# Optimization experiments

Hardware: AMD Instinct MI355X
Metric: run time of the kernel (lower is better)

Reference implementation:

```python
import jax, jax.numpy as jnp
import numpy as np

B, T, H, POOL, MAX_ITER = 32, 1024, 128, 16, 4
D = 2 * H  # feature size of U rows


def _maxout(x, w, b, out_dim, pool):
    # x: [..., fin], w: [fin, out_dim*pool], b: [out_dim*pool]
    y = x @ w + b
    y = y.reshape(y.shape[:-1] + (out_dim, pool))
    return y.max(axis=-1)


def _hmn(U, us, ue, h, WDw, WDb, W1w, W1b, W2w, W2b, W3w, W3b):
    # U: [B,T,2H]; us, ue: [B,2H]; h: [B,H] -> scores [B,T]
    r = jnp.tanh(jnp.concatenate([h, us, ue], axis=-1) @ WDw + WDb)  # [B,H]
    rt = jnp.broadcast_to(r[:, None, :], (U.shape[0], U.shape[1], r.shape[-1]))
    m1 = _maxout(jnp.concatenate([U, rt], axis=-1), W1w, W1b, H, POOL)  # [B,T,H]
    m2 = _maxout(m1, W2w, W2b, H, POOL)                                  # [B,T,H]
    m3 = _maxout(jnp.concatenate([m1, m2], axis=-1), W3w, W3b, 1, POOL)  # [B,T,1]
    return m3[..., 0]  # [B,T]


def _lstm_cell(x, h, c, wih, whh, bih, bhh):
    gates = x @ wih.T + bih + h @ whh.T + bhh  # [B,4H]
    i, f, g, o = jnp.split(gates, 4, axis=-1)
    i, f, o = jax.nn.sigmoid(i), jax.nn.sigmoid(f), jax.nn.sigmoid(o)
    g = jnp.tanh(g)
    c2 = f * c + i * g
    h2 = o * jnp.tanh(c2)
    return h2, c2


def setup_inputs() -> dict:
    key = jax.random.key(0)
    ks = jax.random.split(key, 24)
    s = 0.05
    gn = lambda k, shape: (jax.random.normal(k, shape, jnp.float32) * s)
    inp = {"U": jax.random.normal(ks[0], (B, T, D), jnp.float32)}
    for tag, off in (("s", 1), ("e", 9)):
        inp[f"WD{tag}_w"] = gn(ks[off + 0], (5 * H, H))
        inp[f"WD{tag}_b"] = jnp.zeros((H,), jnp.float32)
        inp[f"W1{tag}_w"] = gn(ks[off + 1], (3 * H, H * POOL))
        inp[f"W1{tag}_b"] = jnp.zeros((H * POOL,), jnp.float32)
        inp[f"W2{tag}_w"] = gn(ks[off + 2], (H, H * POOL))
        inp[f"W2{tag}_b"] = jnp.zeros((H * POOL,), jnp.float32)
        inp[f"W3{tag}_w"] = gn(ks[off + 3], (2 * H, POOL))
        inp[f"W3{tag}_b"] = jnp.zeros((POOL,), jnp.float32)
    inp["lstm_wih"] = gn(ks[20], (4 * H, 4 * H))
    inp["lstm_whh"] = gn(ks[21], (4 * H, H))
    inp["lstm_bih"] = jnp.zeros((4 * H,), jnp.float32)
    inp["lstm_bhh"] = jnp.zeros((4 * H,), jnp.float32)
    return inp


def reference(U,
              WDs_w, WDs_b, W1s_w, W1s_b, W2s_w, W2s_b, W3s_w, W3s_b,
              WDe_w, WDe_b, W1e_w, W1e_b, W2e_w, W2e_b, W3e_w, W3e_b,
              lstm_wih, lstm_whh, lstm_bih, lstm_bhh):
    b = U.shape[0]
    bidx = jnp.arange(b)
    h = jnp.zeros((b, H), U.dtype)
    c = jnp.zeros((b, H), U.dtype)
    us, ue = U[:, 0, :], U[:, 1, :]
    entropies = []
    for _ in range(MAX_ITER):  # training-mode: run all iterations (no host-sync early stop)
        alpha_sc = _hmn(U, us, ue, h, WDs_w, WDs_b, W1s_w, W1s_b, W2s_w, W2s_b, W3s_w, W3s_b)
        alpha = jnp.argmax(alpha_sc, axis=1)           # [B]
        us = U[bidx, alpha, :]                          # data-dependent gather
        beta_sc = _hmn(U, us, ue, h, WDe_w, WDe_b, W1e_w, W1e_b, W2e_w, W2e_b, W3e_w, W3e_b)
        beta = jnp.argmax(beta_sc, axis=1)
        ue = U[bidx, beta, :]
        h, c = _lstm_cell(jnp.concatenate([us, ue], axis=1), h, c,
                          lstm_wih, lstm_whh, lstm_bih, lstm_bhh)
        entropies.append(jnp.stack([alpha_sc, beta_sc], axis=0))
    ent = jnp.stack(entropies, axis=0)  # [max_iter, 2, B, T]
    return alpha, beta, ent
```

## Files before the change

kernel.cpp:

```cpp
#include <hip/hip_runtime.h>
#include <math.h>

static constexpr int cB = 32;
static constexpr int cT = 1024;
static constexpr int cH = 128;
static constexpr int cD = 256;
static constexpr int cN = 2048;
static constexpr int cM = cB * cT;

typedef __attribute__((ext_vector_type(8))) short short8;
typedef __attribute__((ext_vector_type(4))) float f32x4;

__device__ __forceinline__ ushort f2bf(float x) {
    union { float f; unsigned u; } v; v.f = x;
    unsigned r = v.u + 0x7FFF + ((v.u >> 16) & 1);
    return (ushort)(r >> 16);
}
__device__ __forceinline__ float bf2f(ushort h) {
    union { float f; unsigned u; } v; v.u = ((unsigned)h) << 16;
    return v.f;
}

__device__ __forceinline__ void gload_lds16(const ushort* g, ushort* l) {
    __builtin_amdgcn_global_load_lds(
        (const __attribute__((address_space(1))) unsigned int*)(const void*)g,
        (__attribute__((address_space(3))) unsigned int*)(void*)l,
        16, 0, 0);
}

template<int K, bool POOL, bool WRITE_HL>
__global__ __launch_bounds__(256, 2)
void mfma_gemm(const ushort* __restrict__ Ah, const ushort* __restrict__ Al,
               const ushort* __restrict__ Bth, const ushort* __restrict__ Btl,
               const float* __restrict__ initv, int init_bstride,
               float* __restrict__ out, ushort* __restrict__ outh,
               ushort* __restrict__ outl)
{
    __shared__ __attribute__((aligned(16))) ushort sAh[128 * 32];
    __shared__ __attribute__((aligned(16))) ushort sAl[128 * 32];
    __shared__ __attribute__((aligned(16))) ushort sBh[128 * 32];
    __shared__ __attribute__((aligned(16))) ushort sBl[128 * 32];

    const int tid  = threadIdx.x;
    const int wave = tid >> 6;
    const int lane = tid & 63;
    const int l15  = lane & 15;
    const int lg   = lane >> 4;
    const int wr   = wave >> 1;
    const int wc   = wave & 1;
    const int m0   = blockIdx.y * 128;
    const int n0   = blockIdx.x * 128;
    const int brow = m0 >> 10;

    float iv[4] = {0.f, 0.f, 0.f, 0.f};
    if (initv) {
        #pragma unroll
        for (int nf = 0; nf < 4; ++nf)
            iv[nf] = initv[(size_t)brow * init_bstride + n0 + wc * 64 + nf * 16 + l15];
    }

    f32x4 acc[4][4];
    #pragma unroll
    for (int mf = 0; mf < 4; ++mf)
        #pragma unroll
        for (int nf = 0; nf < 4; ++nf)
            acc[mf][nf] = (f32x4){0.f, 0.f, 0.f, 0.f};

    const int st_row_in = lane >> 2;
    const int st_pos    = lane & 3;

    for (int kc = 0; kc < K; kc += 32) {
        #pragma unroll
        for (int q = 0; q < 4; ++q) {
            const ushort* gsrc = (q == 0) ? Ah : (q == 1) ? Al : (q == 2) ? Bth : Btl;
            ushort* lbase = (q == 0) ? sAh : (q == 1) ? sAl : (q == 2) ? sBh : sBl;
            const int rb = (q < 2) ? m0 : n0;
            #pragma unroll
            for (int i2 = 0; i2 < 2; ++i2) {
                int i   = wave * 2 + i2;
                int row = i * 16 + st_row_in;
                int cl  = st_pos ^ (row & 3);
                gload_lds16(gsrc + (size_t)(rb + row) * K + kc + cl * 8,
                            lbase + i * 512);
            }
        }
        __syncthreads();

        short8 a_h[4], a_l[4], b_h[4], b_l[4];
        #pragma unroll
        for (int mf = 0; mf < 4; ++mf) {
            int row  = wr * 64 + mf * 16 + l15;
            int addr = row * 32 + ((lg ^ (row & 3)) * 8);
            a_h[mf] = *(const short8*)(sAh + addr);
            a_l[mf] = *(const short8*)(sAl + addr);
        }
        #pragma unroll
        for (int nf = 0; nf < 4; ++nf) {
            int row  = wc * 64 + nf * 16 + l15;
            int addr = row * 32 + ((lg ^ (row & 3)) * 8);
            b_h[nf] = *(const short8*)(sBh + addr);
            b_l[nf] = *(const short8*)(sBl + addr);
        }

        #pragma unroll
        for (int mf = 0; mf < 4; ++mf)
            #pragma unroll
            for (int nf = 0; nf < 4; ++nf) {
                acc[mf][nf] = __builtin_amdgcn_mfma_f32_16x16x32_bf16(
                    a_h[mf], b_h[nf], acc[mf][nf], 0, 0, 0);
                acc[mf][nf] = __builtin_amdgcn_mfma_f32_16x16x32_bf16(
                    a_h[mf], b_l[nf], acc[mf][nf], 0, 0, 0);
                acc[mf][nf] = __builtin_amdgcn_mfma_f32_16x16x32_bf16(
                    a_l[mf], b_h[nf], acc[mf][nf], 0, 0, 0);
            }
        __syncthreads();
    }

    if (POOL) {
        const int NP = 128;
        #pragma unroll
        for (int mf = 0; mf < 4; ++mf)
            #pragma unroll
            for (int nf = 0; nf < 4; ++nf)
                #pragma unroll
                for (int r = 0; r < 4; ++r) {
                    float v = acc[mf][nf][r] + iv[nf];
                    v = fmaxf(v, __shfl_xor(v, 1));
                    v = fmaxf(v, __shfl_xor(v, 2));
                    v = fmaxf(v, __shfl_xor(v, 4));
                    v = fmaxf(v, __shfl_xor(v, 8));
                    if (l15 == nf) {
                        int row = m0 + wr * 64 + mf * 16 + lg * 4 + r;
                        int col = ((n0 + wc * 64) >> 4) + nf;
                        size_t o = (size_t)row * NP + col;
                        out[o] = v;
                        if (WRITE_HL) {
                            ushort hb = f2bf(v);
                            outh[o] = hb;
                            outl[o] = f2bf(v - bf2f(hb));
                        }
                    }
                }
    } else {
        #pragma unroll
        for (int mf = 0; mf < 4; ++mf)
            #pragma unroll
            for (int nf = 0; nf < 4; ++nf) {
                int col = n0 + wc * 64 + nf * 16 + l15;
                #pragma unroll
                for (int r = 0; r < 4; ++r) {
                    int row = m0 + wr * 64 + mf * 16 + lg * 4 + r;
                    out[(size_t)row * cN + col] = acc[mf][nf][r] + iv[nf];
                }
            }
    }
}

__global__ void m1_from_a1_kernel(const float* __restrict__ A1,
                                  const float* __restrict__ rterm,
                                  float* __restrict__ m1,
                                  ushort* __restrict__ m1h,
                                  ushort* __restrict__ m1l)
{
    int idx = blockIdx.x * 256 + threadIdx.x;
    int m = idx >> 7;
    int o = idx & 127;
    int b = m >> 10;
    const float4* a  = (const float4*)(A1 + (size_t)m * cN + o * 16);
    const float4* rt = (const float4*)(rterm + (size_t)b * cN + o * 16);
    float mx = -3.4e38f;
    #pragma unroll
    for (int q = 0; q < 4; ++q) {
        float4 av = a[q];
        float4 rv = rt[q];
        mx = fmaxf(mx, fmaxf(fmaxf(av.x + rv.x, av.y + rv.y),
                             fmaxf(av.z + rv.z, av.w + rv.w)));
    }
    m1[idx] = mx;
    ushort hb = f2bf(mx);
    m1h[idx] = hb;
    m1l[idx] = f2bf(mx - bf2f(hb));
}

__global__ void wsplit_kernel(const float* __restrict__ W, int K, int N,
                              ushort* __restrict__ th, ushort* __restrict__ tl)
{
    int idx = blockIdx.x * 256 + threadIdx.x;
    if (idx >= K * N) return;
    int k = idx / N, n = idx - k * N;
    float x = W[idx];
    ushort h = f2bf(x);
    th[(size_t)n * K + k] = h;
    tl[(size_t)n * K + k] = f2bf(x - bf2f(h));
}

__global__ void usplit_kernel(const float* __restrict__ U,
                              ushort* __restrict__ uh, ushort* __restrict__ ul)
{
    int idx = blockIdx.x * 256 + threadIdx.x;
    float x = U[idx];
    ushort h = f2bf(x);
    uh[idx] = h;
    ul[idx] = f2bf(x - bf2f(h));
}

__global__ void r_kernel(const float* __restrict__ h, const float* __restrict__ us,
                         const float* __restrict__ ue,
                         const float* __restrict__ WDw, const float* __restrict__ WDb,
                         float* __restrict__ r)
{
    int b = blockIdx.x;
    int j = threadIdx.x;
    __shared__ float x[640];
    x[j]       = h[b * cH + j];
    x[128 + j] = us[b * cD + j];
    x[256 + j] = us[b * cD + 128 + j];
    x[384 + j] = ue[b * cD + j];
    x[512 + j] = ue[b * cD + 128 + j];
    __syncthreads();
    float s = WDb[j];
    for (int k = 0; k < 640; ++k) s = fmaf(x[k], WDw[(size_t)k * cH + j], s);
    r[b * cH + j] = tanhf(s);
}

__global__ void rterm_kernel(const float* __restrict__ r, const float* __restrict__ W1r,
                             const float* __restrict__ W1b, float* __restrict__ rterm)
{
    int b = blockIdx.y;
    int n = blockIdx.x * 256 + threadIdx.x;
    __shared__ float rs[128];
    if (threadIdx.x < 128) rs[threadIdx.x] = r[b * cH + threadIdx.x];
    __syncthreads();
    float s = W1b[n];
    for (int k = 0; k < 128; ++k) s = fmaf(rs[k], W1r[(size_t)k * cN + n], s);
    rterm[(size_t)b * cN + n] = s;
}

__global__ __launch_bounds__(256)
void score_kernel(const float* __restrict__ m1, const float* __restrict__ m2,
                  const float* __restrict__ W3w, const float* __restrict__ W3b,
                  float* __restrict__ ent)
{
    __shared__ float xs[16][257];
    __shared__ float wsh[256 * 16];
    int tid = threadIdx.x;
    int m0 = blockIdx.x * 16;
    #pragma unroll
    for (int q = 0; q < 16; ++q) wsh[tid + q * 256] = W3w[tid + q * 256];
    #pragma unroll
    for (int q = 0; q < 8; ++q) {
        int f = tid + q * 256;
        int rl = f >> 7, col = f & 127;
        xs[rl][col]       = m1[(size_t)(m0 + rl) * cH + col];
        xs[rl][128 + col] = m2[(size_t)(m0 + rl) * cH + col];
    }
    __syncthreads();
    int rl = tid >> 4, p = tid & 15;
    float s = W3b[p];
    for (int k = 0; k < 256; ++k) s = fmaf(xs[rl][k], wsh[k * 16 + p], s);
    #pragma unroll
    for (int off = 8; off; off >>= 1) s = fmaxf(s, __shfl_xor(s, off));
    if (p == 0) ent[m0 + rl] = s;
}

__global__ void argmax_kernel(const float* __restrict__ sc, const float* __restrict__ U,
                              float* __restrict__ uvec, float* __restrict__ outidx)
{
    int b = blockIdx.x;
    int tid = threadIdx.x;
    float bv = -3.4e38f;
    int bi = 0x7fffffff;
    for (int t = tid; t < cT; t += 256) {
        float v = sc[b * cT + t];
        if (v > bv || (v == bv && t < bi)) { bv = v; bi = t; }
    }
    __shared__ float vs[256];
    __shared__ int   is[256];
    vs[tid] = bv; is[tid] = bi;
    __syncthreads();
    for (int s = 128; s > 0; s >>= 1) {
        if (tid < s) {
            if (vs[tid + s] > vs[tid] ||
                (vs[tid + s] == vs[tid] && is[tid + s] < is[tid])) {
                vs[tid] = vs[tid + s];
                is[tid] = is[tid + s];
            }
        }
        __syncthreads();
    }
    int best = is[0];
    if (tid == 0) outidx[b] = (float)best;
    uvec[b * cD + tid % cD] = U[((size_t)b * cT + best) * cD + (tid % cD)];
}

__global__ void lstm_kernel(const float* __restrict__ us, const float* __restrict__ ue,
                            float* __restrict__ h, float* __restrict__ c,
                            const float* __restrict__ wih, const float* __restrict__ whh,
                            const float* __restrict__ bih, const float* __restrict__ bhh)
{
    int b = blockIdx.x;
    int j = threadIdx.x;
    __shared__ float x[512];
    __shared__ float hh[128];
    x[j]       = us[b * cD + j];
    x[128 + j] = us[b * cD + 128 + j];
    x[256 + j] = ue[b * cD + j];
    x[384 + j] = ue[b * cD + 128 + j];
    hh[j] = h[b * cH + j];
    __syncthreads();
    float g4[4];
    #pragma unroll
    for (int gi = 0; gi < 4; ++gi) {
        int row = gi * 128 + j;
        float s = bih[row] + bhh[row];
        const float* wr = wih + (size_t)row * 512;
        for (int k = 0; k < 512; ++k) s = fmaf(x[k], wr[k], s);
        const float* wr2 = whh + (size_t)row * 128;
        for (int k = 0; k < 128; ++k) s = fmaf(hh[k], wr2[k], s);
        g4[gi] = s;
    }
    float i_ = 1.f / (1.f + expf(-g4[0]));
    float f_ = 1.f / (1.f + expf(-g4[1]));
    float g_ = tanhf(g4[2]);
    float o_ = 1.f / (1.f + expf(-g4[3]));
    float c2 = f_ * c[b * cH + j] + i_ * g_;
    float h2 = o_ * tanhf(c2);
    c[b * cH + j] = c2;
    h[b * cH + j] = h2;
}

__global__ void init_kernel(const float* __restrict__ U, float* __restrict__ us,
                            float* __restrict__ ue, float* __restrict__ h,
                            float* __restrict__ c)
{
    int i = blockIdx.x * 256 + threadIdx.x;
    if (i < cB * cD) {
        int b = i >> 8, d = i & 255;
        us[i] = U[((size_t)b * cT + 0) * cD + d];
        ue[i] = U[((size_t)b * cT + 1) * cD + d];
    }
    if (i < cB * cH) { h[i] = 0.f; c[i] = 0.f; }
}

extern "C" void kernel_launch(void* const* d_in, const int* in_sizes, int n_in,
                              void* d_out, int out_size, void* d_ws, size_t ws_size,
                              hipStream_t stream)
{
    const float* U = (const float*)d_in[0];
    const float* WD_w[2] = {(const float*)d_in[1], (const float*)d_in[9]};
    const float* WD_b[2] = {(const float*)d_in[2], (const float*)d_in[10]};
    const float* W1_w[2] = {(const float*)d_in[3], (const float*)d_in[11]};
    const float* W1_b[2] = {(const float*)d_in[4], (const float*)d_in[12]};
    const float* W2_w[2] = {(const float*)d_in[5], (const float*)d_in[13]};
    const float* W2_b[2] = {(const float*)d_in[6], (const float*)d_in[14]};
    const float* W3_w[2] = {(const float*)d_in[7], (const float*)d_in[15]};
    const float* W3_b[2] = {(const float*)d_in[8], (const float*)d_in[16]};
    const float* wih = (const float*)d_in[17];
    const float* whh = (const float*)d_in[18];
    const float* bih = (const float*)d_in[19];
    const float* bhh = (const float*)d_in[20];

    float* ws = (float*)d_ws;
    float* m1 = ws;
    float* m2 = m1 + (size_t)cM * cH;
    float* us = m2 + (size_t)cM * cH;
    float* ue = us + cB * cD;
    float* h  = ue + cB * cD;
    float* c  = h + cB * cH;
    float* r  = c + cB * cH;
    float* rterm = r + cB * cH;
    float* cur = rterm + (size_t)cB * cN;

    ushort* m1h = (ushort*)cur;                   cur += (size_t)cM * cH / 2;
    ushort* m1l = (ushort*)cur;                   cur += (size_t)cM * cH / 2;
    ushort* Uh  = (ushort*)cur;                   cur += (size_t)cM * cD / 2;
    ushort* Ul  = (ushort*)cur;                   cur += (size_t)cM * cD / 2;
    ushort* W1th[2], *W1tl[2], *W2th[2], *W2tl[2];
    for (int sd = 0; sd < 2; ++sd) {
        W1th[sd] = (ushort*)cur; cur += (size_t)cN * cD / 2;
        W1tl[sd] = (ushort*)cur; cur += (size_t)cN * cD / 2;
        W2th[sd] = (ushort*)cur; cur += (size_t)cN * cH / 2;
        W2tl[sd] = (ushort*)cur; cur += (size_t)cN * cH / 2;
    }
    float* A1[2];
    A1[0] = cur;
    A1[1] = A1[0] + (size_t)cM * cN;
    size_t need = (size_t)(A1[1] - ws) + (size_t)cM * cN;
    bool pre = ws_size >= need * sizeof(float);

    float* outf = (float*)d_out;

    init_kernel<<<32, 256, 0, stream>>>(U, us, ue, h, c);
    usplit_kernel<<<(cM * cD) / 256, 256, 0, stream>>>(U, Uh, Ul);
    for (int sd = 0; sd < 2; ++sd) {
        wsplit_kernel<<<(cD * cN) / 256, 256, 0, stream>>>(
            W1_w[sd], cD, cN, W1th[sd], W1tl[sd]);
        wsplit_kernel<<<(cH * cN) / 256, 256, 0, stream>>>(
            W2_w[sd], cH, cN, W2th[sd], W2tl[sd]);
    }

    dim3 ggrid(cN / 128, cM / 128);
    if (pre) {
        for (int sd = 0; sd < 2; ++sd)
            mfma_gemm<256, false, false><<<ggrid, 256, 0, stream>>>(
                Uh, Ul, W1th[sd], W1tl[sd], nullptr, 0, A1[sd], nullptr, nullptr);
    }

    for (int it = 0; it < 4; ++it) {
        for (int sd = 0; sd < 2; ++sd) {
            r_kernel<<<32, 128, 0, stream>>>(h, us, ue, WD_w[sd], WD_b[sd], r);
            rterm_kernel<<<dim3(8, 32), 256, 0, stream>>>(
                r, W1_w[sd] + (size_t)256 * cN, W1_b[sd], rterm);
            if (pre) {
                m1_from_a1_kernel<<<16384, 256, 0, stream>>>(
                    A1[sd], rterm, m1, m1h, m1l);
            } else {
                mfma_gemm<256, true, true><<<ggrid, 256, 0, stream>>>(
                    Uh, Ul, W1th[sd], W1tl[sd], rterm, cN, m1, m1h, m1l);
            }
            mfma_gemm<128, true, false><<<ggrid, 256, 0, stream>>>(
                m1h, m1l, W2th[sd], W2tl[sd], W2_b[sd], 0, m2, nullptr, nullptr);
            float* ent = outf + 64 + (size_t)(it * 2 + sd) * cB * cT;
            score_kernel<<<2048, 256, 0, stream>>>(m1, m2, W3_w[sd], W3_b[sd], ent);
            argmax_kernel<<<32, 256, 0, stream>>>(ent, U, sd ? ue : us,
                                                  outf + (sd ? 32 : 0));
        }
        lstm_kernel<<<32, 128, 0, stream>>>(us, ue, h, c, wih, whh, bih, bhh);
    }
}
```

Baseline: 2.887 ms.

## Load GEMM B operand directly from global, remap grid for XCD locality

The mfma_gemm kernel stops staging the B (weight) tiles in LDS. Each wave now reads its B fragments straight from global memory into registers, which halves LDS use and drops the LDS writes and reads for B. The launch grid becomes 1D with a block-index remap that groups tiles by blockIdx modulo 8, so each XCD works on neighbouring tiles and shares L2. The A-tile LDS swizzle also changes from row&3 to (row>>1)&3 to cut bank conflicts. The risk is that B global loads are not shared across the two waves in a row pair and may add latency and L2 traffic.

After: 3.310 ms. 14.7% more time.

```diff
diff --git a/kernel.cpp b/kernel.cpp
--- a/kernel.cpp
+++ b/kernel.cpp
@@ -38,8 +38,6 @@
 {
     __shared__ __attribute__((aligned(16))) ushort sAh[128 * 32];
     __shared__ __attribute__((aligned(16))) ushort sAl[128 * 32];
-    __shared__ __attribute__((aligned(16))) ushort sBh[128 * 32];
-    __shared__ __attribute__((aligned(16))) ushort sBl[128 * 32];
 
     const int tid  = threadIdx.x;
     const int wave = tid >> 6;
@@ -48,8 +46,13 @@
     const int lg   = lane >> 4;
     const int wr   = wave >> 1;
     const int wc   = wave & 1;
-    const int m0   = blockIdx.y * 128;
-    const int n0   = blockIdx.x * 128;
+
+    const int wg  = blockIdx.x;
+    const int lin = (wg & 7) * 512 + (wg >> 3);
+    const int bx  = lin & 15;
+    const int by  = lin >> 4;
+    const int m0  = by * 128;
+    const int n0  = bx * 128;
     const int brow = m0 >> 10;
 
     float iv[4] = {0.f, 0.f, 0.f, 0.f};
@@ -66,40 +69,36 @@
         for (int nf = 0; nf < 4; ++nf)
             acc[mf][nf] = (f32x4){0.f, 0.f, 0.f, 0.f};
 
-    const int st_row_in = lane >> 2;
-    const int st_pos    = lane & 3;
-
     for (int kc = 0; kc < K; kc += 32) {
         #pragma unroll
-        for (int q = 0; q < 4; ++q) {
-            const ushort* gsrc = (q == 0) ? Ah : (q == 1) ? Al : (q == 2) ? Bth : Btl;
-            ushort* lbase = (q == 0) ? sAh : (q == 1) ? sAl : (q == 2) ? sBh : sBl;
-            const int rb = (q < 2) ? m0 : n0;
+        for (int q = 0; q < 2; ++q) {
+            const ushort* gsrc = q ? Al : Ah;
+            ushort* lbase = q ? sAl : sAh;
             #pragma unroll
             for (int i2 = 0; i2 < 2; ++i2) {
                 int i   = wave * 2 + i2;
-                int row = i * 16 + st_row_in;
-                int cl  = st_pos ^ (row & 3);
-                gload_lds16(gsrc + (size_t)(rb + row) * K + kc + cl * 8,
+                int row = i * 16 + (lane >> 2);
+                int cl  = (lane & 3) ^ ((row >> 1) & 3);
+                gload_lds16(gsrc + (size_t)(m0 + row) * K + kc + cl * 8,
                             lbase + i * 512);
             }
         }
+        short8 b_h[4], b_l[4];
+        #pragma unroll
+        for (int nf = 0; nf < 4; ++nf) {
+            size_t off = (size_t)(n0 + wc * 64 + nf * 16 + l15) * K + kc + lg * 8;
+            b_h[nf] = *(const short8*)(Bth + off);
+            b_l[nf] = *(const short8*)(Btl + off);
+        }
         __syncthreads();
 
-        short8 a_h[4], a_l[4], b_h[4], b_l[4];
+        short8 a_h[4], a_l[4];
         #pragma unroll
         for (int mf = 0; mf < 4; ++mf) {
             int row  = wr * 64 + mf * 16 + l15;
-            int addr = row * 32 + ((lg ^ (row & 3)) * 8);
+            int addr = row * 32 + ((lg ^ ((row >> 1) & 3)) * 8);
             a_h[mf] = *(const short8*)(sAh + addr);
             a_l[mf] = *(const short8*)(sAl + addr);
-        }
-        #pragma unroll
-        for (int nf = 0; nf < 4; ++nf) {
-            int row  = wc * 64 + nf * 16 + l15;
-            int addr = row * 32 + ((lg ^ (row & 3)) * 8);
-            b_h[nf] = *(const short8*)(sBh + addr);
-            b_l[nf] = *(const short8*)(sBl + addr);
         }
 
         #pragma unroll
@@ -399,7 +398,7 @@
             W2_w[sd], cH, cN, W2th[sd], W2tl[sd]);
     }
 
-    dim3 ggrid(cN / 128, cM / 128);
+    const int ggrid = (cN / 128) * (cM / 128);
     if (pre) {
         for (int sd = 0; sd < 2; ++sd)
             mfma_gemm<256, false, false><<<ggrid, 256, 0, stream>>>(
```
